# Kernel optimization log

Measured on AMD Instinct MI355X. Metric: run time of the kernel, lower is better.

## Reference

```python
import jax, jax.numpy as jnp
import numpy as np

IMAGE_W = 1024
IMAGE_H = 1024
MIN_SCORE_THRESHOLD = 0.05
NMS_THRESHOLD = 0.5
MAX_DETECTION_NUM = 100


def setup_inputs() -> dict:
    key = jax.random.key(0)
    k1, k2, k3, k4 = jax.random.split(key, 4)
    B, N, C = 2, 8192, 80
    cls_heads = jax.random.uniform(k1, (B, N, C), jnp.float32)          # post-sigmoid class probs
    reg_heads = jax.random.normal(k2, (B, N, 4), jnp.float32)           # tx,ty,tw,th
    ctr = jax.random.uniform(k3, (B, N, 2), jnp.float32, 0.0, 1024.0)   # anchor centers
    wh = jax.random.uniform(k4, (B, N, 2), jnp.float32, 16.0, 256.0)    # anchor sizes
    anchors = jnp.concatenate([ctr - 0.5 * wh, ctr + 0.5 * wh], axis=-1)  # x1,y1,x2,y2
    return {"cls_heads": cls_heads, "reg_heads": reg_heads, "anchors": anchors}


def _snap_boxes(reg, anchors):
    # reg, anchors: [N, 4]
    awh = anchors[:, 2:] - anchors[:, :2]
    actr = anchors[:, :2] + 0.5 * awh
    factor = jnp.array([0.1, 0.1, 0.2, 0.2], dtype=reg.dtype)
    reg = reg * factor
    pwh = jnp.exp(reg[:, 2:]) * awh
    pctr = reg[:, :2] * awh + actr
    boxes = jnp.concatenate([pctr - 0.5 * pwh, pctr + 0.5 * pwh], axis=1)
    boxes = jax.lax.stop_gradient(boxes).astype(jnp.int32)  # torch .int() truncation
    boxes = boxes.at[:, 0].set(jnp.maximum(boxes[:, 0], 0))
    boxes = boxes.at[:, 1].set(jnp.maximum(boxes[:, 1], 0))
    boxes = boxes.at[:, 2].set(jnp.minimum(boxes[:, 2], IMAGE_W - 1))
    boxes = boxes.at[:, 3].set(jnp.minimum(boxes[:, 3], IMAGE_H - 1))
    return boxes


def _decode_one(cls_head, reg_head, anchor):
    # cls_head: [N, C], reg_head: [N, 4], anchor: [N, 4]
    scores = jnp.max(cls_head, axis=-1)
    classes = jnp.argmax(cls_head, axis=-1).astype(jnp.int32)
    boxes = _snap_boxes(reg_head, anchor)  # int32 [N,4]
    valid = scores > MIN_SCORE_THRESHOLD

    order = jnp.argsort(-scores)  # descending score order
    s = scores[order]
    c = classes[order]
    b = boxes[order]
    v = valid[order]

    bf = b.astype(jnp.float32)
    x1, y1, x2, y2 = bf[:, 0], bf[:, 1], bf[:, 2], bf[:, 3]
    area = jnp.maximum(x2 - x1, 0.0) * jnp.maximum(y2 - y1, 0.0)
    ix1 = jnp.maximum(x1[:, None], x1[None, :])
    iy1 = jnp.maximum(y1[:, None], y1[None, :])
    ix2 = jnp.minimum(x2[:, None], x2[None, :])
    iy2 = jnp.minimum(y2[:, None], y2[None, :])
    inter = jnp.maximum(ix2 - ix1, 0.0) * jnp.maximum(iy2 - iy1, 0.0)
    union = area[:, None] + area[None, :] - inter
    iou = jnp.where(union > 0.0, inter / union, 0.0)  # [N,N]

    N = s.shape[0]
    idx = jnp.arange(N)
    # class-wise suppression: box j (lower score) suppressed by kept box i if IoU>thr
    sup = (iou > NMS_THRESHOLD) & (c[:, None] == c[None, :]) & (idx[None, :] > idx[:, None])

    def body(i, keep):
        return jnp.where(keep[i], keep & ~sup[i], keep)

    keep = jax.lax.fori_loop(0, N, body, v)

    final_scores = jnp.where(keep, s, -1.0)
    top_s, top_i = jax.lax.top_k(final_scores, MAX_DETECTION_NUM)
    ok = top_s > -0.5
    out_scores = jnp.where(ok, top_s, -1.0)
    out_classes = jnp.where(ok, c[top_i], -1)
    out_boxes = jnp.where(ok[:, None], b[top_i], -1)
    return out_scores, out_classes, out_boxes


def reference(cls_heads, reg_heads, anchors):
    # cls_heads: [B,N,C], reg_heads: [B,N,4], anchors: [B,N,4]
    return jax.vmap(_decode_one)(cls_heads, reg_heads, anchors)
```

## Files before the change

### kernel.cpp

```cpp
#include <hip/hip_runtime.h>
#include <stdint.h>

#define NANCH   8192
#define NCLS    80
#define IMW     1024
#define IMH     1024
#define MAXDET  100
#define SCORE_TH 0.05f
#define TAU      0.999691f
#define CAP      512
#define KSENT    0x7FFFFFF0
#define ROWS_PB  128
#define LSTRIDE  84

__device__ __forceinline__ float key_score(uint64_t key) {
    uint32_t m = (uint32_t)(key >> 32);
    uint32_t bits = (m & 0x80000000u) ? (m & 0x7FFFFFFFu) : ~m;
    return __uint_as_float(bits);
}

__global__ __launch_bounds__(256)
void decode_kernel(const float* __restrict__ cls_heads,
                   const float* __restrict__ reg_heads,
                   const float* __restrict__ anchors,
                   int* __restrict__ cnt,
                   uint64_t* __restrict__ wk,
                   uint64_t* __restrict__ wm,
                   ulonglong2* __restrict__ surv) {
    __shared__ float slab[ROWS_PB * LSTRIDE];

    const int tid  = threadIdx.x;
    const int lane = tid & 63;
    const int b    = blockIdx.y;
    const int r0   = blockIdx.x * ROWS_PB;

    {
        const float* gbase = cls_heads + ((size_t)b * NANCH + r0) * NCLS;
#pragma unroll
        for (int it = 0; it < (ROWS_PB * NCLS) / (256 * 4); ++it) {
            int g = it * 1024 + tid * 4;
            float4 v = *reinterpret_cast<const float4*>(gbase + g);
            int row = g / NCLS, col = g % NCLS;
            *reinterpret_cast<float4*>(&slab[row * LSTRIDE + col]) = v;
        }
    }
    __syncthreads();

    if (tid >= ROWS_PB) return;

    const int n   = r0 + tid;
    const int row = b * NANCH + n;

    float best = -1e30f; int bestj = 0;
    {
        const float4* rp = reinterpret_cast<const float4*>(&slab[tid * LSTRIDE]);
#pragma unroll
        for (int k = 0; k < NCLS / 4; ++k) {
            float4 v = rp[k];
            if (v.x > best) { best = v.x; bestj = 4 * k + 0; }
            if (v.y > best) { best = v.y; bestj = 4 * k + 1; }
            if (v.z > best) { best = v.z; bestj = 4 * k + 2; }
            if (v.w > best) { best = v.w; bestj = 4 * k + 3; }
        }
    }

    float4 r = reinterpret_cast<const float4*>(reg_heads)[row];
    float4 a = reinterpret_cast<const float4*>(anchors)[row];

    float awx = __fsub_rn(a.z, a.x);
    float awy = __fsub_rn(a.w, a.y);
    float acx = __fadd_rn(a.x, __fmul_rn(0.5f, awx));
    float acy = __fadd_rn(a.y, __fmul_rn(0.5f, awy));
    float rx = __fmul_rn(r.x, 0.1f);
    float ry = __fmul_rn(r.y, 0.1f);
    float rw = __fmul_rn(r.z, 0.2f);
    float rh = __fmul_rn(r.w, 0.2f);
    float pwx = __fmul_rn(expf(rw), awx);
    float pwy = __fmul_rn(expf(rh), awy);
    float pcx = __fadd_rn(__fmul_rn(rx, awx), acx);
    float pcy = __fadd_rn(__fmul_rn(ry, awy), acy);

    int x1 = (int)__fsub_rn(pcx, __fmul_rn(0.5f, pwx));
    int y1 = (int)__fsub_rn(pcy, __fmul_rn(0.5f, pwy));
    int x2 = (int)__fadd_rn(pcx, __fmul_rn(0.5f, pwx));
    int y2 = (int)__fadd_rn(pcy, __fmul_rn(0.5f, pwy));
    x1 = max(x1, 0);
    y1 = max(y1, 0);
    x2 = min(x2, IMW - 1);
    y2 = min(y2, IMH - 1);

    uint32_t u = __float_as_uint(best);
    uint32_t mono = (u & 0x80000000u) ? ~u : (u | 0x80000000u);
    uint64_t key = ((uint64_t)mono << 32)
                 | ((uint64_t)((~(uint32_t)n) & 0xFFFFu) << 16)
                 | (uint64_t)(uint32_t)bestj;
    uint64_t meta = (uint64_t)(uint16_t)x1
                  | ((uint64_t)(uint16_t)y1 << 16)
                  | ((uint64_t)(uint16_t)x2 << 32)
                  | ((uint64_t)(uint16_t)y2 << 48);

    wk[row] = key;
    wm[row] = meta;

    bool svv = (best > TAU);
    uint64_t mask = __ballot(svv);
    int rank = __popcll(mask & ((1ULL << lane) - 1ULL));
    int base = 0;
    if (lane == 0 && mask) base = atomicAdd(cnt + b, __popcll(mask));
    base = __shfl(base, 0);
    if (svv) {
        int p = base + rank;
        if (p < CAP) surv[(size_t)b * CAP + p] = make_ulonglong2(key, meta);
    }
}

struct Kept {
    float x1[2], y1[2], x2[2], y2[2], ar[2];
    int   cl[2];
};

__device__ __forceinline__ void nms_try_keep(uint64_t key, uint64_t meta, float s,
                                             int lane, int& nk, Kept& K,
                                             float* __restrict__ out, int b) {
    int cls = (int)(key & 0xFFFFu);
    float cx1 = (float)(short)(meta & 0xFFFFu);
    float cy1 = (float)(short)((meta >> 16) & 0xFFFFu);
    float cx2 = (float)(short)((meta >> 32) & 0xFFFFu);
    float cy2 = (float)(short)((meta >> 48) & 0xFFFFu);
    float ca = fmaxf(cx2 - cx1, 0.f) * fmaxf(cy2 - cy1, 0.f);

    bool supp = false;
#pragma unroll
    for (int r = 0; r < 2; ++r) {
        int slot = lane + 64 * r;
        if (slot < nk && K.cl[r] == cls) {
            float ix1 = fmaxf(K.x1[r], cx1), iy1 = fmaxf(K.y1[r], cy1);
            float ix2 = fminf(K.x2[r], cx2), iy2 = fminf(K.y2[r], cy2);
            float inter = fmaxf(ix2 - ix1, 0.f) * fmaxf(iy2 - iy1, 0.f);
            if (3.f * inter > K.ar[r] + ca) supp = true;
        }
    }
    if (__ballot(supp) != 0ULL) return;

    int rr = nk >> 6, l = nk & 63;
    if (lane == l) {
        if (rr == 0) { K.x1[0]=cx1; K.y1[0]=cy1; K.x2[0]=cx2; K.y2[0]=cy2; K.ar[0]=ca; K.cl[0]=cls; }
        else         { K.x1[1]=cx1; K.y1[1]=cy1; K.x2[1]=cx2; K.y2[1]=cy2; K.ar[1]=ca; K.cl[1]=cls; }
    }
    if (lane == 0) {
        out[b * MAXDET + nk] = s;
        out[2 * MAXDET + b * MAXDET + nk] = (float)cls;
        float* ob = out + 4 * MAXDET + (size_t)(b * MAXDET + nk) * 4;
        ob[0] = cx1; ob[1] = cy1; ob[2] = cx2; ob[3] = cy2;
    }
    ++nk;
}

__global__ __launch_bounds__(256)
void sort_nms_kernel(const int* __restrict__ cnt,
                     const uint64_t* __restrict__ wk,
                     const uint64_t* __restrict__ wm,
                     const ulonglong2* __restrict__ surv,
                     float* __restrict__ out) {
    __shared__ __align__(16) ulonglong2 sv_[CAP];
    __shared__ __align__(16) ulonglong2 sq[CAP];
    __shared__ __align__(16) uint64_t skey[CAP + 16];
    __shared__ float4 kept_box[128];
    __shared__ float  kept_area[128];
    __shared__ int    kept_cls[128];
    __shared__ uint64_t smask[4];
    __shared__ uint64_t sby[4 * 64];
    __shared__ int snk, sdone, sneedfb;
    __shared__ uint64_t fbmap[NANCH / 64];

    const int b = blockIdx.x;
    const int tid = threadIdx.x;
    const int lane = tid & 63;
    const int w = tid >> 6;

    int c = cnt[b];
    bool overflow = (c > CAP) || (c < 0);
    if (overflow) c = 0;
    const int cpad   = (c + 63) & ~63;
    const int cpad16 = (c + 15) & ~15;

    if (tid < 128) kept_cls[tid] = KSENT;
    if (tid == 0) { snk = 0; sdone = 0; sneedfb = overflow ? 1 : 0; }

    for (int i = tid; i < c; i += 256) {
        ulonglong2 v = surv[(size_t)b * CAP + i];
        sv_[i] = v; skey[i] = v.x;
    }
    for (int i = c + tid; i < cpad16; i += 256) skey[i] = 0ULL;
    __syncthreads();

    for (int i = tid; i < c; i += 256) {
        uint64_t ky = skey[i];
        int r = 0;
        for (int j0 = 0; j0 < cpad16; j0 += 16) {
            int acc = 0;
#pragma unroll
            for (int u = 0; u < 8; ++u) {
                ulonglong2 pr = *reinterpret_cast<const ulonglong2*>(&skey[j0 + 2 * u]);
                acc += (int)(pr.x > ky) + (int)(pr.y > ky);
            }
            r += acc;
        }
        sq[r] = sv_[i];
    }
    for (int i = c + tid; i < cpad; i += 256) sq[i] = make_ulonglong2(0ULL, 0ULL);

    for (int p0 = 0; p0 < cpad; p0 += 64) {
        __syncthreads();
        if (sdone) break;
        const int nk = snk;

        ulonglong2 kv = sq[p0 + lane];
        uint64_t key = kv.x, meta = kv.y;
        float s = key_score(key);
        bool sval = (s > SCORE_TH);
        int cls_c = sval ? (int)(key & 0xFFFFu) : -1;
        float cx1 = (float)(short)(meta & 0xFFFFu);
        float cy1 = (float)(short)((meta >> 16) & 0xFFFFu);
        float cx2 = (float)(short)((meta >> 32) & 0xFFFFu);
        float cy2 = (float)(short)((meta >> 48) & 0xFFFFu);
        float ca = fmaxf(cx2 - cx1, 0.f) * fmaxf(cy2 - cy1, 0.f);

        bool supk = false;
        int kp = (((nk + 3) >> 2) + 7) & ~7;
        for (int k0 = 0; k0 < kp; k0 += 8) {
#pragma unroll
            for (int u = 0; u < 8; ++u) {
                int j = w + 4 * (k0 + u);
                float4 kb = kept_box[j];
                float ka = kept_area[j];
                int kc = kept_cls[j];
                float ix1 = fmaxf(kb.x, cx1), iy1 = fmaxf(kb.y, cy1);
                float ix2 = fminf(kb.z, cx2), iy2 = fminf(kb.w, cy2);
                float inter = fmaxf(ix2 - ix1, 0.f) * fmaxf(iy2 - iy1, 0.f);
                supk |= (kc == cls_c) & (3.f * inter > ka + ca);
            }
        }

        uint64_t sbyw = 0;
#pragma unroll
        for (int u = 0; u < 16; ++u) {
            int t = (w << 4) + u;
            ulonglong2 tv = sq[p0 + t];
            uint64_t tkey = tv.x, tmeta = tv.y;
            float ts = key_score(tkey);
            int tcls = (int)(tkey & 0xFFFFu);
            float tx1 = (float)(short)(tmeta & 0xFFFFu);
            float ty1 = (float)(short)((tmeta >> 16) & 0xFFFFu);
            float tx2 = (float)(short)((tmeta >> 32) & 0xFFFFu);
            float ty2 = (float)(short)((tmeta >> 48) & 0xFFFFu);
            float ta = fmaxf(tx2 - tx1, 0.f) * fmaxf(ty2 - ty1, 0.f);
            float ix1 = fmaxf(tx1, cx1), iy1 = fmaxf(ty1, cy1);
            float ix2 = fminf(tx2, cx2), iy2 = fminf(ty2, cy2);
            float inter = fmaxf(ix2 - ix1, 0.f) * fmaxf(iy2 - iy1, 0.f);
            bool sup = (t < lane) && (ts > SCORE_TH) && (tcls == cls_c)
                       && (3.f * inter > ta + ca);
            sbyw |= ((uint64_t)sup) << t;
        }

        uint64_t mk = __ballot(supk);
        if (lane == 0) smask[w] = mk;
        sby[(w << 6) + lane] = sbyw;
        __syncthreads();

        if (w == 0) {
            uint64_t supkAll = smask[0] | smask[1] | smask[2] | smask[3];
            uint64_t supBy = sby[lane] | sby[64 + lane] | sby[128 + lane] | sby[192 + lane];
            bool alive0 = sval && !((supkAll >> lane) & 1ULL);

            uint64_t aliveCand = __ballot(alive0);
            uint64_t aliveMask;
            if (__ballot(supBy != 0ULL) == 0ULL) {
                aliveMask = aliveCand;
            } else {
                uint64_t killed = 0;
                for (int t = 0; t < 64; ++t) {
                    uint64_t kill_t = __ballot((supBy >> t) & 1ULL);
                    bool talive = ((aliveCand >> t) & 1ULL) && !((killed >> t) & 1ULL);
                    if (talive) killed |= kill_t;
                }
                aliveMask = aliveCand & ~killed;
            }

            int myrank = __popcll(aliveMask & ((1ULL << lane) - 1ULL));
            bool keepme = ((aliveMask >> lane) & 1ULL) && (nk + myrank < MAXDET);
            if (keepme) {
                int slot = nk + myrank;
                kept_box[slot]  = make_float4(cx1, cy1, cx2, cy2);
                kept_area[slot] = ca;
                kept_cls[slot]  = cls_c;
                out[b * MAXDET + slot] = s;
                out[2 * MAXDET + b * MAXDET + slot] = (float)cls_c;
                float* ob = out + 4 * MAXDET + (size_t)(b * MAXDET + slot) * 4;
                ob[0] = cx1; ob[1] = cy1; ob[2] = cx2; ob[3] = cy2;
            }
            int navail = __popcll(aliveMask);
            int room = MAXDET - nk;
            int nk2 = nk + ((navail < room) ? navail : room);
            uint64_t invalid = __ballot(!sval);
            if (lane == 0) {
                snk = nk2;
                if (nk2 >= MAXDET) sdone = 1;
                else if (invalid) { sneedfb = 1; sdone = 1; }
            }
        }
    }
    __syncthreads();

    int nk = snk;
    bool need_fb = sneedfb || (!sdone && nk < MAXDET);

    if (tid >= 64) return;

    if (need_fb) {
        const uint64_t* wkb = wk + (size_t)b * NANCH;
        const uint64_t* wmb = wm + (size_t)b * NANCH;
        for (int i = lane; i < NANCH / 64; i += 64) fbmap[i] = 0ULL;
        __builtin_amdgcn_wave_barrier();

        nk = 0;
        Kept K;
        K.cl[0] = K.cl[1] = -1;
        K.x1[0]=K.y1[0]=K.x2[0]=K.y2[0]=K.ar[0]=0.f;
        K.x1[1]=K.y1[1]=K.x2[1]=K.y2[1]=K.ar[1]=0.f;

        for (int iter = 0; iter < NANCH; ++iter) {
            uint64_t mybest = 0; int myq = -1;
            for (int q = lane; q < NANCH; q += 64) {
                bool cons = (fbmap[q >> 6] >> (q & 63)) & 1ULL;
                uint64_t kk = wkb[q];
                if (!cons && kk > mybest) { mybest = kk; myq = q; }
            }
            uint64_t best = mybest;
#pragma unroll
            for (int j = 32; j; j >>= 1) {
                uint64_t o = __shfl_xor(best, j);
                if (o > best) best = o;
            }
            if (best == 0ULL) break;
            float s = key_score(best);
            if (!(s > SCORE_TH)) break;
            uint64_t msk = __ballot(mybest == best);
            int wl = __ffsll((unsigned long long)msk) - 1;
            int q = __shfl(myq, wl);
            if (lane == wl) fbmap[q >> 6] |= (1ULL << (q & 63));
            uint64_t cm = wmb[q];
            nms_try_keep(best, cm, s, lane, nk, K, out, b);
            if (nk == MAXDET) break;
            __builtin_amdgcn_wave_barrier();
        }
    }

    for (int t = nk + lane; t < MAXDET; t += 64) {
        out[b * MAXDET + t] = -1.f;
        out[2 * MAXDET + b * MAXDET + t] = -1.f;
        float* ob = out + 4 * MAXDET + (size_t)(b * MAXDET + t) * 4;
        ob[0] = -1.f; ob[1] = -1.f; ob[2] = -1.f; ob[3] = -1.f;
    }
}

extern "C" void kernel_launch(void* const* d_in, const int* in_sizes, int n_in,
                              void* d_out, int out_size, void* d_ws, size_t ws_size,
                              hipStream_t stream) {
    (void)in_sizes; (void)n_in; (void)out_size; (void)ws_size;
    const float* cls_heads = (const float*)d_in[0];
    const float* reg_heads = (const float*)d_in[1];
    const float* anchors   = (const float*)d_in[2];
    float* out = (float*)d_out;

    char* w = (char*)d_ws;
    int*        cnt  = (int*)w;
    uint64_t*   wk   = (uint64_t*)(w + 1024);
    uint64_t*   wm   = (uint64_t*)(w + 1024 + 131072);
    ulonglong2* surv = (ulonglong2*)(w + 1024 + 262144);

    hipMemsetAsync(cnt, 0, 2 * sizeof(int), stream);
    decode_kernel<<<dim3(NANCH / ROWS_PB, 2), 256, 0, stream>>>(cls_heads, reg_heads, anchors,
                                                                cnt, wk, wm, surv);
    sort_nms_kernel<<<dim3(2), 256, 0, stream>>>(cnt, wk, wm, surv, out);
}
```

Measured before the change: 23.63 us.

## Split class argmax across four lanes per anchor and prefetch survivors unconditionally

```diff
diff --git a/kernel.cpp b/kernel.cpp
--- a/kernel.cpp
+++ b/kernel.cpp
@@ -10,8 +10,7 @@
 #define TAU      0.999691f
 #define CAP      512
 #define KSENT    0x7FFFFFF0
-#define ROWS_PB  128
-#define LSTRIDE  84
+#define ROWS_PB  64
 
 __device__ __forceinline__ float key_score(uint64_t key) {
     uint32_t m = (uint32_t)(key >> 32);
@@ -27,82 +26,82 @@
                    uint64_t* __restrict__ wk,
                    uint64_t* __restrict__ wm,
                    ulonglong2* __restrict__ surv) {
-    __shared__ float slab[ROWS_PB * LSTRIDE];
-
     const int tid  = threadIdx.x;
     const int lane = tid & 63;
+    const int part = tid & 3;
     const int b    = blockIdx.y;
-    const int r0   = blockIdx.x * ROWS_PB;
-
-    {
-        const float* gbase = cls_heads + ((size_t)b * NANCH + r0) * NCLS;
-#pragma unroll
-        for (int it = 0; it < (ROWS_PB * NCLS) / (256 * 4); ++it) {
-            int g = it * 1024 + tid * 4;
-            float4 v = *reinterpret_cast<const float4*>(gbase + g);
-            int row = g / NCLS, col = g % NCLS;
-            *reinterpret_cast<float4*>(&slab[row * LSTRIDE + col]) = v;
-        }
-    }
-    __syncthreads();
-
-    if (tid >= ROWS_PB) return;
-
-    const int n   = r0 + tid;
-    const int row = b * NANCH + n;
+    const int n    = blockIdx.x * ROWS_PB + (tid >> 2);
+    const int row  = b * NANCH + n;
 
     float best = -1e30f; int bestj = 0;
     {
-        const float4* rp = reinterpret_cast<const float4*>(&slab[tid * LSTRIDE]);
-#pragma unroll
-        for (int k = 0; k < NCLS / 4; ++k) {
-            float4 v = rp[k];
-            if (v.x > best) { best = v.x; bestj = 4 * k + 0; }
-            if (v.y > best) { best = v.y; bestj = 4 * k + 1; }
-            if (v.z > best) { best = v.z; bestj = 4 * k + 2; }
-            if (v.w > best) { best = v.w; bestj = 4 * k + 3; }
-        }
-    }
-
-    float4 r = reinterpret_cast<const float4*>(reg_heads)[row];
-    float4 a = reinterpret_cast<const float4*>(anchors)[row];
-
-    float awx = __fsub_rn(a.z, a.x);
-    float awy = __fsub_rn(a.w, a.y);
-    float acx = __fadd_rn(a.x, __fmul_rn(0.5f, awx));
-    float acy = __fadd_rn(a.y, __fmul_rn(0.5f, awy));
-    float rx = __fmul_rn(r.x, 0.1f);
-    float ry = __fmul_rn(r.y, 0.1f);
-    float rw = __fmul_rn(r.z, 0.2f);
-    float rh = __fmul_rn(r.w, 0.2f);
-    float pwx = __fmul_rn(expf(rw), awx);
-    float pwy = __fmul_rn(expf(rh), awy);
-    float pcx = __fadd_rn(__fmul_rn(rx, awx), acx);
-    float pcy = __fadd_rn(__fmul_rn(ry, awy), acy);
-
-    int x1 = (int)__fsub_rn(pcx, __fmul_rn(0.5f, pwx));
-    int y1 = (int)__fsub_rn(pcy, __fmul_rn(0.5f, pwy));
-    int x2 = (int)__fadd_rn(pcx, __fmul_rn(0.5f, pwx));
-    int y2 = (int)__fadd_rn(pcy, __fmul_rn(0.5f, pwy));
-    x1 = max(x1, 0);
-    y1 = max(y1, 0);
-    x2 = min(x2, IMW - 1);
-    y2 = min(y2, IMH - 1);
-
-    uint32_t u = __float_as_uint(best);
-    uint32_t mono = (u & 0x80000000u) ? ~u : (u | 0x80000000u);
-    uint64_t key = ((uint64_t)mono << 32)
-                 | ((uint64_t)((~(uint32_t)n) & 0xFFFFu) << 16)
-                 | (uint64_t)(uint32_t)bestj;
-    uint64_t meta = (uint64_t)(uint16_t)x1
-                  | ((uint64_t)(uint16_t)y1 << 16)
-                  | ((uint64_t)(uint16_t)x2 << 32)
-                  | ((uint64_t)(uint16_t)y2 << 48);
-
-    wk[row] = key;
-    wm[row] = meta;
-
-    bool svv = (best > TAU);
+        const float* rp = cls_heads + (size_t)row * NCLS;
+#pragma unroll
+        for (int k = 0; k < 5; ++k) {
+            int j0 = part * 4 + k * 16;
+            float4 v = *reinterpret_cast<const float4*>(rp + j0);
+            if (v.x > best) { best = v.x; bestj = j0 + 0; }
+            if (v.y > best) { best = v.y; bestj = j0 + 1; }
+            if (v.z > best) { best = v.z; bestj = j0 + 2; }
+            if (v.w > best) { best = v.w; bestj = j0 + 3; }
+        }
+    }
+
+    uint32_t ub = __float_as_uint(best);
+    uint32_t mono = (ub & 0x80000000u) ? ~ub : (ub | 0x80000000u);
+    uint64_t kk = ((uint64_t)mono << 8) | (uint64_t)(255 - bestj);
+    {
+        uint64_t o = __shfl_xor(kk, 1); if (o > kk) kk = o;
+        o = __shfl_xor(kk, 2); if (o > kk) kk = o;
+    }
+
+    bool owner = (part == 0);
+    uint32_t mono32 = (uint32_t)(kk >> 8);
+    int bj = 255 - (int)(kk & 0xFF);
+
+    uint64_t key = 0, meta = 0;
+    bool svv = false;
+    if (owner) {
+        float4 r = reinterpret_cast<const float4*>(reg_heads)[row];
+        float4 a = reinterpret_cast<const float4*>(anchors)[row];
+
+        float awx = __fsub_rn(a.z, a.x);
+        float awy = __fsub_rn(a.w, a.y);
+        float acx = __fadd_rn(a.x, __fmul_rn(0.5f, awx));
+        float acy = __fadd_rn(a.y, __fmul_rn(0.5f, awy));
+        float rx = __fmul_rn(r.x, 0.1f);
+        float ry = __fmul_rn(r.y, 0.1f);
+        float rw = __fmul_rn(r.z, 0.2f);
+        float rh = __fmul_rn(r.w, 0.2f);
+        float pwx = __fmul_rn(expf(rw), awx);
+        float pwy = __fmul_rn(expf(rh), awy);
+        float pcx = __fadd_rn(__fmul_rn(rx, awx), acx);
+        float pcy = __fadd_rn(__fmul_rn(ry, awy), acy);
+
+        int x1 = (int)__fsub_rn(pcx, __fmul_rn(0.5f, pwx));
+        int y1 = (int)__fsub_rn(pcy, __fmul_rn(0.5f, pwy));
+        int x2 = (int)__fadd_rn(pcx, __fmul_rn(0.5f, pwx));
+        int y2 = (int)__fadd_rn(pcy, __fmul_rn(0.5f, pwy));
+        x1 = max(x1, 0);
+        y1 = max(y1, 0);
+        x2 = min(x2, IMW - 1);
+        y2 = min(y2, IMH - 1);
+
+        key = ((uint64_t)mono32 << 32)
+            | ((uint64_t)((~(uint32_t)n) & 0xFFFFu) << 16)
+            | (uint64_t)(uint32_t)bj;
+        meta = (uint64_t)(uint16_t)x1
+             | ((uint64_t)(uint16_t)y1 << 16)
+             | ((uint64_t)(uint16_t)x2 << 32)
+             | ((uint64_t)(uint16_t)y2 << 48);
+
+        wk[row] = key;
+        wm[row] = meta;
+
+        uint32_t mono_tau = __float_as_uint(TAU) | 0x80000000u;
+        svv = (mono32 > mono_tau);
+    }
+
     uint64_t mask = __ballot(svv);
     int rank = __popcll(mask & ((1ULL << lane) - 1ULL));
     int base = 0;
@@ -178,20 +177,19 @@
     const int lane = tid & 63;
     const int w = tid >> 6;
 
+    ulonglong2 v0 = surv[(size_t)b * CAP + tid];
+    ulonglong2 v1 = surv[(size_t)b * CAP + 256 + tid];
     int c = cnt[b];
+
     bool overflow = (c > CAP) || (c < 0);
     if (overflow) c = 0;
     const int cpad   = (c + 63) & ~63;
     const int cpad16 = (c + 15) & ~15;
 
+    sv_[tid]       = v0;  skey[tid]       = (tid < c)       ? v0.x : 0ULL;
+    sv_[256 + tid] = v1;  skey[256 + tid] = (256 + tid < c) ? v1.x : 0ULL;
     if (tid < 128) kept_cls[tid] = KSENT;
     if (tid == 0) { snk = 0; sdone = 0; sneedfb = overflow ? 1 : 0; }
-
-    for (int i = tid; i < c; i += 256) {
-        ulonglong2 v = surv[(size_t)b * CAP + i];
-        sv_[i] = v; skey[i] = v.x;
-    }
-    for (int i = c + tid; i < cpad16; i += 256) skey[i] = 0ULL;
     __syncthreads();
 
     for (int i = tid; i < c; i += 256) {
@@ -333,8 +331,8 @@
             uint64_t mybest = 0; int myq = -1;
             for (int q = lane; q < NANCH; q += 64) {
                 bool cons = (fbmap[q >> 6] >> (q & 63)) & 1ULL;
-                uint64_t kk = wkb[q];
-                if (!cons && kk > mybest) { mybest = kk; myq = q; }
+                uint64_t kk2 = wkb[q];
+                if (!cons && kk2 > mybest) { mybest = kk2; myq = q; }
             }
             uint64_t best = mybest;
 #pragma unroll
```

Result: slower. 24.21 us (+2.4%).
